# Performance work log

Measured on AMD Instinct MI355X. Metric: run time of the kernel, lower is better.

Reference implementation:

```python
import jax, jax.numpy as jnp
import numpy as np

B, L, D, E, H, TOPK = 4, 2048, 1024, 8, 4096, 2


def setup_inputs() -> dict:
    key = jax.random.key(0)
    k0, k1, k2, k3 = jax.random.split(key, 4)
    x = jax.random.normal(k0, (B, L, D), dtype=jnp.float32)
    Wr = jax.random.normal(k1, (D, E), dtype=jnp.float32) * 0.02
    W1 = jax.random.normal(k2, (E, D, H), dtype=jnp.float32) * 0.02
    W2 = jax.random.normal(k3, (E, H, D), dtype=jnp.float32) * 0.02
    return {"x": x, "Wr": Wr, "W1": W1, "W2": W2, "top_k": TOPK}


def reference(x, Wr, W1, W2, top_k):
    # x: (B, L, D) -> flatten tokens
    b, l, d = x.shape
    e = Wr.shape[1]
    xf = x.reshape(b * l, d)                                  # (T, D)

    # Router: softmax over experts, top-k, renormalize selected weights
    probs = jax.nn.softmax(xf @ Wr, axis=-1)                  # (T, E)
    w, idx = jax.lax.top_k(probs, top_k)                      # (T, K)
    w = w / jnp.sum(w, axis=-1, keepdims=True)

    # Dense per-token-per-expert weight; unrouted experts get weight 0,
    # which is mathematically identical to the masked gather/scatter loop.
    w_full = jnp.sum(jax.nn.one_hot(idx, e, dtype=xf.dtype) * w[..., None], axis=1)  # (T, E)

    # Expert MLPs (Linear -> SiLU -> Linear), batched over experts
    h = jax.nn.silu(jnp.einsum('td,edh->teh', xf, W1))        # (T, E, H)
    y = jnp.einsum('teh,ehd->ted', h, W2)                     # (T, E, D)

    # Weighted combine over experts
    out = jnp.einsum('ted,te->td', y, w_full)                 # (T, D)
    return out.reshape(b, l, d)
```

## Files before the change

### kernel.cpp

```cpp
#include <hip/hip_runtime.h>
#include <hip/hip_bf16.h>


#define TOK  8192
#define DDIM 1024
#define NEXP 8
#define HDIM 4096

typedef __attribute__((ext_vector_type(8))) _Float16 f16x8;
typedef __attribute__((ext_vector_type(4))) float    f32x4;

static constexpr size_t OFF_COUNTS  = 0;
static constexpr size_t OFF_TOKENS  = 4096;
static constexpr size_t OFF_WEIGHTS = OFF_TOKENS + (size_t)NEXP * TOK * 4;
static constexpr size_t OFF_SLOTS   = OFF_WEIGHTS + (size_t)NEXP * TOK * 4;
static constexpr size_t OFF_H       = 1ull << 20;
static constexpr size_t OFF_Y       = OFF_H + (1ull << 27);

__global__ __launch_bounds__(256) void router_k(
    const float* __restrict__ x, const float* __restrict__ Wr,
    int* __restrict__ counts, int* __restrict__ tokens, float* __restrict__ weights,
    int* __restrict__ slots) {
  const int lane = threadIdx.x & 63;
  const int t = blockIdx.x * 4 + (threadIdx.x >> 6);
  const float* xr = x + (size_t)t * DDIM;

  float acc[NEXP];
#pragma unroll
  for (int e = 0; e < NEXP; ++e) acc[e] = 0.f;

#pragma unroll
  for (int it = 0; it < DDIM / 256; ++it) {
    const int d = it * 256 + lane * 4;
    const float4 xv = *(const float4*)(xr + d);
    const float* wr = Wr + (size_t)d * NEXP;
#pragma unroll
    for (int j = 0; j < 4; ++j) {
      const float xs = (j == 0) ? xv.x : (j == 1) ? xv.y : (j == 2) ? xv.z : xv.w;
      const float4 w0 = *(const float4*)(wr + j * NEXP);
      const float4 w1 = *(const float4*)(wr + j * NEXP + 4);
      acc[0] = fmaf(xs, w0.x, acc[0]); acc[1] = fmaf(xs, w0.y, acc[1]);
      acc[2] = fmaf(xs, w0.z, acc[2]); acc[3] = fmaf(xs, w0.w, acc[3]);
      acc[4] = fmaf(xs, w1.x, acc[4]); acc[5] = fmaf(xs, w1.y, acc[5]);
      acc[6] = fmaf(xs, w1.z, acc[6]); acc[7] = fmaf(xs, w1.w, acc[7]);
    }
  }
#pragma unroll
  for (int e = 0; e < NEXP; ++e) {
#pragma unroll
    for (int off = 32; off > 0; off >>= 1) acc[e] += __shfl_xor(acc[e], off);
  }
  if (lane == 0) {
    int i0 = 0; float v0 = acc[0];
#pragma unroll
    for (int e = 1; e < NEXP; ++e) if (acc[e] > v0) { v0 = acc[e]; i0 = e; }
    int i1 = -1; float v1 = -3.4e38f;
#pragma unroll
    for (int e = 0; e < NEXP; ++e) if (e != i0 && acc[e] > v1) { v1 = acc[e]; i1 = e; }
    const float r = expf(v1 - v0);
    const float inv = 1.f / (1.f + r);
    const int p0 = atomicAdd(counts + i0 * 64, 1);
    tokens[i0 * TOK + p0] = t; weights[i0 * TOK + p0] = inv;
    const int p1 = atomicAdd(counts + i1 * 64, 1);
    tokens[i1 * TOK + p1] = t; weights[i1 * TOK + p1] = r * inv;
    slots[t * 2]     = (i0 << 16) | p0;
    slots[t * 2 + 1] = (i1 << 16) | p1;
  }
}


template <int LD>
__device__ __forceinline__ void b_load(const float* bP, int kt, float (&bv)[4][4]) {
#pragma unroll
  for (int g = 0; g < 4; ++g)
#pragma unroll
    for (int j = 0; j < 4; ++j)
      bv[g][j] = bP[(size_t)(kt + j) * LD + 32 * g];
}

__device__ __forceinline__ void b_store(int bn, int bk4, const float (&bv)[4][4],
                                        _Float16 (*Bs)[40]) {
#pragma unroll
  for (int g = 0; g < 4; ++g) {
    const unsigned p0 = __builtin_bit_cast(unsigned, __builtin_amdgcn_cvt_pkrtz(bv[g][0], bv[g][1]));
    const unsigned p1 = __builtin_bit_cast(unsigned, __builtin_amdgcn_cvt_pkrtz(bv[g][2], bv[g][3]));
    *(uint2*)&Bs[bn + 32 * g][bk4] = make_uint2(p0, p1);
  }
}

__device__ __forceinline__ void a1_store(const float4 (&av)[4], int ar, int aseg,
                                         _Float16 (*As)[40]) {
  unsigned u[8];
#pragma unroll
  for (int j = 0; j < 4; ++j) {
    u[j * 2]     = __builtin_bit_cast(unsigned, __builtin_amdgcn_cvt_pkrtz(av[j].x, av[j].y));
    u[j * 2 + 1] = __builtin_bit_cast(unsigned, __builtin_amdgcn_cvt_pkrtz(av[j].z, av[j].w));
  }
  *(uint4*)&As[ar][aseg]     = make_uint4(u[0], u[1], u[2], u[3]);
  *(uint4*)&As[ar][aseg + 8] = make_uint4(u[4], u[5], u[6], u[7]);
}

__device__ __forceinline__ void g_compute(const _Float16 (*As)[40], const _Float16 (*Bs)[40],
                                          int wr, int wc, int lane, f32x4 (&acc)[4][4]) {
  const int l15 = lane & 15, g8 = (lane >> 4) * 8;
  f16x8 af[4], bf[4];
#pragma unroll
  for (int mf = 0; mf < 4; ++mf) af[mf] = *(const f16x8*)&As[wr + mf * 16 + l15][g8];
#pragma unroll
  for (int nf = 0; nf < 4; ++nf) bf[nf] = *(const f16x8*)&Bs[wc + nf * 16 + l15][g8];
#pragma unroll
  for (int mf = 0; mf < 4; ++mf)
#pragma unroll
    for (int nf = 0; nf < 4; ++nf)
      acc[mf][nf] = __builtin_amdgcn_mfma_f32_16x16x32_f16(af[mf], bf[nf], acc[mf][nf], 0, 0, 0);
}

__global__ __launch_bounds__(256) void gemm1_k(
    const float* __restrict__ x, const float* __restrict__ W1,
    const int* __restrict__ counts, const int* __restrict__ tokens,
    _Float16* __restrict__ hbuf) {
  const int e = blockIdx.z;
  const int n_e = counts[e * 64];
  const int m0 = blockIdx.y * 128;
  if (m0 >= n_e) return;
  const int n0 = blockIdx.x * 128;
  int off = 0;
#pragma unroll
  for (int i = 0; i < NEXP; ++i) off += (i < e) ? counts[i * 64] : 0;

  __shared__ __align__(16) _Float16 As[2][128][40];
  __shared__ __align__(16) _Float16 Bs[2][128][40];

  const int tid = threadIdx.x, lane = tid & 63, w = tid >> 6;
  const int wr = (w >> 1) * 64, wc = (w & 1) * 64;

  const int ar = tid >> 1, aseg = (tid & 1) * 16;
  const int rA = m0 + ar;
  const int tokA = (rA < n_e) ? tokens[e * TOK + rA] : 0;
  const float* aP = x + (size_t)tokA * DDIM + aseg;
  const int bn = tid & 31, bk4 = (tid >> 5) * 4;
  const float* bP = W1 + (size_t)e * DDIM * HDIM + (size_t)bk4 * HDIM + n0 + bn;

  f32x4 acc[4][4] = {};

  float4 av[4]; float bv[4][4];
#pragma unroll
  for (int j = 0; j < 4; ++j) av[j] = *(const float4*)(aP + j * 4);
  b_load<HDIM>(bP, 0, bv);
  a1_store(av, ar, aseg, As[0]);
  b_store(bn, bk4, bv, Bs[0]);
  __syncthreads();

  int cur = 0;
  for (int t = 0; t < DDIM / 32 - 1; ++t) {
    const int kn = (t + 1) * 32;
#pragma unroll
    for (int j = 0; j < 4; ++j) av[j] = *(const float4*)(aP + kn + j * 4);
    b_load<HDIM>(bP, kn, bv);
    g_compute(As[cur], Bs[cur], wr, wc, lane, acc);
    a1_store(av, ar, aseg, As[cur ^ 1]);
    b_store(bn, bk4, bv, Bs[cur ^ 1]);
    __syncthreads();
    cur ^= 1;
  }
  g_compute(As[cur], Bs[cur], wr, wc, lane, acc);

  const int l15 = lane & 15, rq = (lane >> 4) * 4;
#pragma unroll
  for (int mf = 0; mf < 4; ++mf) {
#pragma unroll
    for (int q = 0; q < 4; ++q) {
      const int r = m0 + wr + mf * 16 + rq + q;
      if (r < n_e) {
        _Float16* hp = hbuf + (size_t)(off + r) * HDIM + n0 + wc + l15;
#pragma unroll
        for (int nf = 0; nf < 4; ++nf) {
          const float v = acc[mf][nf][q];
          hp[nf * 16] = (_Float16)(v / (1.f + __expf(-v)));
        }
      }
    }
  }
}

__global__ __launch_bounds__(256) void gemm2_k(
    const _Float16* __restrict__ hbuf, const float* __restrict__ W2,
    const int* __restrict__ counts, _Float16* __restrict__ ybuf) {
  const int e = blockIdx.z;
  const int n_e = counts[e * 64];
  const int m0 = blockIdx.y * 128;
  if (m0 >= n_e) return;
  const int n0 = blockIdx.x * 128;
  int off = 0;
#pragma unroll
  for (int i = 0; i < NEXP; ++i) off += (i < e) ? counts[i * 64] : 0;

  __shared__ __align__(16) _Float16 As[2][128][40];
  __shared__ __align__(16) _Float16 Bs[2][128][40];

  const int tid = threadIdx.x, lane = tid & 63, w = tid >> 6;
  const int wr = (w >> 1) * 64, wc = (w & 1) * 64;

  const int ar = tid >> 1, aseg = (tid & 1) * 16;
  int rA = m0 + ar; if (rA >= n_e) rA = m0;
  const _Float16* aP = hbuf + (size_t)(off + rA) * HDIM + aseg;
  const int bn = tid & 31, bk4 = (tid >> 5) * 4;
  const float* bP = W2 + (size_t)e * HDIM * DDIM + (size_t)bk4 * DDIM + n0 + bn;

  f32x4 acc[4][4] = {};

  uint4 av[2]; float bv[4][4];
  av[0] = *(const uint4*)(aP); av[1] = *(const uint4*)(aP + 8);
  b_load<DDIM>(bP, 0, bv);
  *(uint4*)&As[0][ar][aseg]     = av[0];
  *(uint4*)&As[0][ar][aseg + 8] = av[1];
  b_store(bn, bk4, bv, Bs[0]);
  __syncthreads();

  int cur = 0;
  for (int t = 0; t < HDIM / 32 - 1; ++t) {
    const int kn = (t + 1) * 32;
    av[0] = *(const uint4*)(aP + kn);
    av[1] = *(const uint4*)(aP + kn + 8);
    b_load<DDIM>(bP, kn, bv);
    g_compute(As[cur], Bs[cur], wr, wc, lane, acc);
    *(uint4*)&As[cur ^ 1][ar][aseg]     = av[0];
    *(uint4*)&As[cur ^ 1][ar][aseg + 8] = av[1];
    b_store(bn, bk4, bv, Bs[cur ^ 1]);
    __syncthreads();
    cur ^= 1;
  }
  g_compute(As[cur], Bs[cur], wr, wc, lane, acc);

  const int l15 = lane & 15, rq = (lane >> 4) * 4;
#pragma unroll
  for (int mf = 0; mf < 4; ++mf) {
#pragma unroll
    for (int q = 0; q < 4; ++q) {
      const int r = m0 + wr + mf * 16 + rq + q;
      if (r < n_e) {
        _Float16* yp = ybuf + (size_t)(off + r) * DDIM + n0 + wc + l15;
#pragma unroll
        for (int nf = 0; nf < 4; ++nf) yp[nf * 16] = (_Float16)acc[mf][nf][q];
      }
    }
  }
}

__global__ __launch_bounds__(256) void combine_k(
    const _Float16* __restrict__ ybuf, const int* __restrict__ counts,
    const int* __restrict__ slots, const float* __restrict__ weights,
    float* __restrict__ out) {
  const int t = blockIdx.x;
  const int s0 = slots[t * 2], s1 = slots[t * 2 + 1];
  const int e0 = s0 >> 16, p0 = s0 & 0xFFFF;
  const int e1 = s1 >> 16, p1 = s1 & 0xFFFF;
  int off0 = 0, off1 = 0;
#pragma unroll
  for (int i = 0; i < NEXP; ++i) {
    const int c = counts[i * 64];
    off0 += (i < e0) ? c : 0;
    off1 += (i < e1) ? c : 0;
  }
  const float w0 = weights[e0 * TOK + p0];
  const float w1 = weights[e1 * TOK + p1];
  const int col = threadIdx.x * 4;
  const ushort4 u0 = *(const ushort4*)(ybuf + (size_t)(off0 + p0) * DDIM + col);
  const ushort4 u1 = *(const ushort4*)(ybuf + (size_t)(off1 + p1) * DDIM + col);
  float4 o;
  o.x = w0 * (float)__builtin_bit_cast(_Float16, u0.x) + w1 * (float)__builtin_bit_cast(_Float16, u1.x);
  o.y = w0 * (float)__builtin_bit_cast(_Float16, u0.y) + w1 * (float)__builtin_bit_cast(_Float16, u1.y);
  o.z = w0 * (float)__builtin_bit_cast(_Float16, u0.z) + w1 * (float)__builtin_bit_cast(_Float16, u1.z);
  o.w = w0 * (float)__builtin_bit_cast(_Float16, u0.w) + w1 * (float)__builtin_bit_cast(_Float16, u1.w);
  *(float4*)(out + (size_t)t * DDIM + col) = o;
}

extern "C" void kernel_launch(void* const* d_in, const int* in_sizes, int n_in,
                              void* d_out, int out_size, void* d_ws, size_t ws_size,
                              hipStream_t stream) {
  const float* x  = (const float*)d_in[0];
  const float* Wr = (const float*)d_in[1];
  const float* W1 = (const float*)d_in[2];
  const float* W2 = (const float*)d_in[3];
  float* out = (float*)d_out;
  char* ws = (char*)d_ws;

  int*      counts  = (int*)(ws + OFF_COUNTS);
  int*      tokens  = (int*)(ws + OFF_TOKENS);
  float*    weights = (float*)(ws + OFF_WEIGHTS);
  int*      slots   = (int*)(ws + OFF_SLOTS);
  _Float16* hbuf    = (_Float16*)(ws + OFF_H);
  _Float16* ybuf    = (_Float16*)(ws + OFF_Y);

  hipMemsetAsync(counts, 0, 2048, stream);

  router_k<<<TOK / 4, 256, 0, stream>>>(x, Wr, counts, tokens, weights, slots);

  const dim3 g1(HDIM / 128, TOK / 128, NEXP);
  const dim3 g2(DDIM / 128, TOK / 128, NEXP);
  gemm1_k<<<g1, 256, 0, stream>>>(x, W1, counts, tokens, hbuf);
  gemm2_k<<<g2, 256, 0, stream>>>(hbuf, W2, counts, ybuf);
  combine_k<<<TOK, 256, 0, stream>>>(ybuf, counts, slots, weights, out);
}
```

Measured before the change: 867.7 us.

## Double M tile to 256 rows with 512-thread blocks in expert GEMMs

Both expert GEMM kernels now use 512-thread blocks covering 256x128 output tiles instead of 256x128-thread tiles. B-tile loading is spread across more threads with two k-rows each, and addressing switches to integer offsets from base pointers. This halves redundant fp32 weight loads per token row and raises work per block. The cost is more LDS per block, fewer blocks for small experts and possibly lower occupancy.

After: 992.9 us. 1.14x slower.

```diff
diff --git a/kernel.cpp b/kernel.cpp
--- a/kernel.cpp
+++ b/kernel.cpp
@@ -70,22 +70,26 @@
 
 
 template <int LD>
-__device__ __forceinline__ void b_load(const float* bP, int kt, float (&bv)[4][4]) {
+__device__ __forceinline__ void b_loadi(const float* __restrict__ Wb, int o, float (&bv)[4][2]) {
 #pragma unroll
   for (int g = 0; g < 4; ++g)
 #pragma unroll
-    for (int j = 0; j < 4; ++j)
-      bv[g][j] = bP[(size_t)(kt + j) * LD + 32 * g];
-}
-
-__device__ __forceinline__ void b_store(int bn, int bk4, const float (&bv)[4][4],
+    for (int j = 0; j < 2; ++j)
+      bv[g][j] = Wb[o + j * LD + 32 * g];
+}
+
+__device__ __forceinline__ void b_store(int bn, int bk2, const float (&bv)[4][2],
                                         _Float16 (*Bs)[40]) {
 #pragma unroll
   for (int g = 0; g < 4; ++g) {
-    const unsigned p0 = __builtin_bit_cast(unsigned, __builtin_amdgcn_cvt_pkrtz(bv[g][0], bv[g][1]));
-    const unsigned p1 = __builtin_bit_cast(unsigned, __builtin_amdgcn_cvt_pkrtz(bv[g][2], bv[g][3]));
-    *(uint2*)&Bs[bn + 32 * g][bk4] = make_uint2(p0, p1);
-  }
+    const unsigned p = __builtin_bit_cast(unsigned, __builtin_amdgcn_cvt_pkrtz(bv[g][0], bv[g][1]));
+    *(unsigned*)&Bs[bn + 32 * g][bk2] = p;
+  }
+}
+
+__device__ __forceinline__ void a_loadi(const float* __restrict__ xb, int o, float4 (&av)[4]) {
+#pragma unroll
+  for (int j = 0; j < 4; ++j) av[j] = *(const float4*)(xb + o + j * 4);
 }
 
 __device__ __forceinline__ void a1_store(const float4 (&av)[4], int ar, int aseg,
@@ -115,20 +119,20 @@
       acc[mf][nf] = __builtin_amdgcn_mfma_f32_16x16x32_f16(af[mf], bf[nf], acc[mf][nf], 0, 0, 0);
 }
 
-__global__ __launch_bounds__(256) void gemm1_k(
+__global__ __launch_bounds__(512) void gemm1_k(
     const float* __restrict__ x, const float* __restrict__ W1,
     const int* __restrict__ counts, const int* __restrict__ tokens,
     _Float16* __restrict__ hbuf) {
   const int e = blockIdx.z;
   const int n_e = counts[e * 64];
-  const int m0 = blockIdx.y * 128;
+  const int m0 = blockIdx.y * 256;
   if (m0 >= n_e) return;
   const int n0 = blockIdx.x * 128;
   int off = 0;
 #pragma unroll
   for (int i = 0; i < NEXP; ++i) off += (i < e) ? counts[i * 64] : 0;
 
-  __shared__ __align__(16) _Float16 As[2][128][40];
+  __shared__ __align__(16) _Float16 As[2][256][40];
   __shared__ __align__(16) _Float16 Bs[2][128][40];
 
   const int tid = threadIdx.x, lane = tid & 63, w = tid >> 6;
@@ -137,29 +141,28 @@
   const int ar = tid >> 1, aseg = (tid & 1) * 16;
   const int rA = m0 + ar;
   const int tokA = (rA < n_e) ? tokens[e * TOK + rA] : 0;
-  const float* aP = x + (size_t)tokA * DDIM + aseg;
-  const int bn = tid & 31, bk4 = (tid >> 5) * 4;
-  const float* bP = W1 + (size_t)e * DDIM * HDIM + (size_t)bk4 * HDIM + n0 + bn;
+  const int ao = tokA * DDIM + aseg;
+  const int bn = tid & 31, bk2 = (tid >> 5) * 2;
+  const float* __restrict__ Wb = W1 + (size_t)e * DDIM * HDIM;
+  const int bo = bk2 * HDIM + n0 + bn;
 
   f32x4 acc[4][4] = {};
 
-  float4 av[4]; float bv[4][4];
-#pragma unroll
-  for (int j = 0; j < 4; ++j) av[j] = *(const float4*)(aP + j * 4);
-  b_load<HDIM>(bP, 0, bv);
+  float4 av[4]; float bv[4][2];
+  a_loadi(x, ao, av);
+  b_loadi<HDIM>(Wb, bo, bv);
   a1_store(av, ar, aseg, As[0]);
-  b_store(bn, bk4, bv, Bs[0]);
+  b_store(bn, bk2, bv, Bs[0]);
   __syncthreads();
 
   int cur = 0;
-  for (int t = 0; t < DDIM / 32 - 1; ++t) {
-    const int kn = (t + 1) * 32;
-#pragma unroll
-    for (int j = 0; j < 4; ++j) av[j] = *(const float4*)(aP + kn + j * 4);
-    b_load<HDIM>(bP, kn, bv);
+  constexpr int NS = DDIM / 32;
+  for (int t = 0; t < NS - 1; ++t) {
+    a_loadi(x, ao + (t + 1) * 32, av);
+    b_loadi<HDIM>(Wb, bo + (t + 1) * 32 * HDIM, bv);
     g_compute(As[cur], Bs[cur], wr, wc, lane, acc);
     a1_store(av, ar, aseg, As[cur ^ 1]);
-    b_store(bn, bk4, bv, Bs[cur ^ 1]);
+    b_store(bn, bk2, bv, Bs[cur ^ 1]);
     __syncthreads();
     cur ^= 1;
   }
@@ -183,19 +186,19 @@
   }
 }
 
-__global__ __launch_bounds__(256) void gemm2_k(
+__global__ __launch_bounds__(512) void gemm2_k(
     const _Float16* __restrict__ hbuf, const float* __restrict__ W2,
     const int* __restrict__ counts, _Float16* __restrict__ ybuf) {
   const int e = blockIdx.z;
   const int n_e = counts[e * 64];
-  const int m0 = blockIdx.y * 128;
+  const int m0 = blockIdx.y * 256;
   if (m0 >= n_e) return;
   const int n0 = blockIdx.x * 128;
   int off = 0;
 #pragma unroll
   for (int i = 0; i < NEXP; ++i) off += (i < e) ? counts[i * 64] : 0;
 
-  __shared__ __align__(16) _Float16 As[2][128][40];
+  __shared__ __align__(16) _Float16 As[2][256][40];
   __shared__ __align__(16) _Float16 Bs[2][128][40];
 
   const int tid = threadIdx.x, lane = tid & 63, w = tid >> 6;
@@ -203,30 +206,31 @@
 
   const int ar = tid >> 1, aseg = (tid & 1) * 16;
   int rA = m0 + ar; if (rA >= n_e) rA = m0;
-  const _Float16* aP = hbuf + (size_t)(off + rA) * HDIM + aseg;
-  const int bn = tid & 31, bk4 = (tid >> 5) * 4;
-  const float* bP = W2 + (size_t)e * HDIM * DDIM + (size_t)bk4 * DDIM + n0 + bn;
+  const int ao = (off + rA) * HDIM + aseg;
+  const int bn = tid & 31, bk2 = (tid >> 5) * 2;
+  const float* __restrict__ Wb = W2 + (size_t)e * HDIM * DDIM;
+  const int bo = bk2 * DDIM + n0 + bn;
 
   f32x4 acc[4][4] = {};
 
-  uint4 av[2]; float bv[4][4];
-  av[0] = *(const uint4*)(aP); av[1] = *(const uint4*)(aP + 8);
-  b_load<DDIM>(bP, 0, bv);
-  *(uint4*)&As[0][ar][aseg]     = av[0];
-  *(uint4*)&As[0][ar][aseg + 8] = av[1];
-  b_store(bn, bk4, bv, Bs[0]);
+  uint4 av[2]; float bv[4][2];
+  av[0] = *(const uint4*)(hbuf + ao);
+  av[1] = *(const uint4*)(hbuf + ao + 8);
+  b_loadi<DDIM>(Wb, bo, bv);
+  *(uint4*)&As[0][ar][aseg] = av[0]; *(uint4*)&As[0][ar][aseg + 8] = av[1];
+  b_store(bn, bk2, bv, Bs[0]);
   __syncthreads();
 
   int cur = 0;
-  for (int t = 0; t < HDIM / 32 - 1; ++t) {
+  constexpr int NS = HDIM / 32;
+  for (int t = 0; t < NS - 1; ++t) {
     const int kn = (t + 1) * 32;
-    av[0] = *(const uint4*)(aP + kn);
-    av[1] = *(const uint4*)(aP + kn + 8);
-    b_load<DDIM>(bP, kn, bv);
+    av[0] = *(const uint4*)(hbuf + ao + kn);
+    av[1] = *(const uint4*)(hbuf + ao + kn + 8);
+    b_loadi<DDIM>(Wb, bo + kn * DDIM, bv);
     g_compute(As[cur], Bs[cur], wr, wc, lane, acc);
-    *(uint4*)&As[cur ^ 1][ar][aseg]     = av[0];
-    *(uint4*)&As[cur ^ 1][ar][aseg + 8] = av[1];
-    b_store(bn, bk4, bv, Bs[cur ^ 1]);
+    *(uint4*)&As[cur ^ 1][ar][aseg] = av[0]; *(uint4*)&As[cur ^ 1][ar][aseg + 8] = av[1];
+    b_store(bn, bk2, bv, Bs[cur ^ 1]);
     __syncthreads();
     cur ^= 1;
   }
@@ -296,9 +300,9 @@
 
   router_k<<<TOK / 4, 256, 0, stream>>>(x, Wr, counts, tokens, weights, slots);
 
-  const dim3 g1(HDIM / 128, TOK / 128, NEXP);
-  const dim3 g2(DDIM / 128, TOK / 128, NEXP);
-  gemm1_k<<<g1, 256, 0, stream>>>(x, W1, counts, tokens, hbuf);
-  gemm2_k<<<g2, 256, 0, stream>>>(hbuf, W2, counts, ybuf);
+  const dim3 g1(HDIM / 128, TOK / 256, NEXP);
+  const dim3 g2(DDIM / 128, TOK / 256, NEXP);
+  gemm1_k<<<g1, 512, 0, stream>>>(x, W1, counts, tokens, hbuf);
+  gemm2_k<<<g2, 512, 0, stream>>>(hbuf, W2, counts, ybuf);
   combine_k<<<TOK, 256, 0, stream>>>(ybuf, counts, slots, weights, out);
 }
```
